# Kernel tuning notes

Measured on AMD Instinct MI355X. Metric: run time of the kernel, lower is better.

Reference implementation:

```python
import jax, jax.numpy as jnp
import numpy as np

def setup_inputs() -> dict:
    key = jax.random.key(0)
    k1, k2, k3 = jax.random.split(key, 3)
    N, G, D = 500000, 10000, 128
    n_embedding = jax.random.normal(k1, (N, D), dtype=jnp.float32)
    g_embedding = jax.random.normal(k2, (G, D), dtype=jnp.float32)
    n_batch = jnp.sort(jax.random.randint(k3, (N,), 0, G, dtype=jnp.int64))
    return {"n_embedding": n_embedding, "g_embedding": g_embedding,
            "n_batch": n_batch, "size": G}

def reference(n_embedding, g_embedding, n_batch, size):
    # gather graph embedding per node: [N, D]
    g_per_node = g_embedding[n_batch]
    # sigmoid of per-node dot product: [N]
    coefs = jax.nn.sigmoid(jnp.sum(n_embedding * g_per_node, axis=1))
    # weighted nodes scatter-added into per-graph pooled output: [G, D]
    weighted = coefs[:, None] * n_embedding
    return jax.ops.segment_sum(weighted, n_batch, num_segments=size)
```

## Files before the change

### kernel.cpp

```cpp
#include <hip/hip_runtime.h>
#include <math.h>


#define BLOCK_THREADS 256
#define GRID_BLOCKS   2048
#define U 4

__global__ __launch_bounds__(BLOCK_THREADS)
void n2g_attention_kernel(const float* __restrict__ n_emb,
                          const float* __restrict__ g_emb,
                          const int*   __restrict__ n_batch,
                          float* __restrict__ out,
                          int N)
{
    const int hw_in_block = threadIdx.x >> 5;
    const int hw_id       = blockIdx.x * (BLOCK_THREADS >> 5) + hw_in_block;
    const int l32         = threadIdx.x & 31;
    const int col         = l32 * 4;
    const int num_hw      = GRID_BLOCKS * (BLOCK_THREADS >> 5);

    const int per   = (N + num_hw - 1) / num_hw;
    const int start = hw_id * per;
    const int end   = min(start + per, N);
    if (start >= N) return;

    float4 acc = make_float4(0.f, 0.f, 0.f, 0.f);
    int cur_g = n_batch[start];

    int i = start;

    for (; i + U <= end; i += U) {
        int    gj[U];
        float4 nv[U], gv[U];

        #pragma unroll
        for (int j = 0; j < U; ++j) gj[j] = n_batch[i + j];
        #pragma unroll
        for (int j = 0; j < U; ++j)
            nv[j] = *(const float4*)(n_emb + (size_t)(i + j) * 128 + col);
        #pragma unroll
        for (int j = 0; j < U; ++j)
            gv[j] = *(const float4*)(g_emb + (size_t)gj[j] * 128 + col);

        float d[U];
        #pragma unroll
        for (int j = 0; j < U; ++j)
            d[j] = nv[j].x * gv[j].x + nv[j].y * gv[j].y
                 + nv[j].z * gv[j].z + nv[j].w * gv[j].w;

        #pragma unroll
        for (int m = 1; m <= 16; m <<= 1) {
            #pragma unroll
            for (int j = 0; j < U; ++j)
                d[j] += __shfl_xor(d[j], m, 64);
        }

        #pragma unroll
        for (int j = 0; j < U; ++j) {
            const float c = 1.0f / (1.0f + __expf(-d[j]));
            if (gj[j] != cur_g) {
                atomicAdd(&out[(size_t)cur_g * 128 + col + 0], acc.x);
                atomicAdd(&out[(size_t)cur_g * 128 + col + 1], acc.y);
                atomicAdd(&out[(size_t)cur_g * 128 + col + 2], acc.z);
                atomicAdd(&out[(size_t)cur_g * 128 + col + 3], acc.w);
                acc = make_float4(0.f, 0.f, 0.f, 0.f);
                cur_g = gj[j];
            }
            acc.x += c * nv[j].x;
            acc.y += c * nv[j].y;
            acc.z += c * nv[j].z;
            acc.w += c * nv[j].w;
        }
    }

    for (; i < end; ++i) {
        const int g = n_batch[i];
        const float4 nv = *(const float4*)(n_emb + (size_t)i * 128 + col);
        const float4 gv = *(const float4*)(g_emb + (size_t)g * 128 + col);
        float d = nv.x * gv.x + nv.y * gv.y + nv.z * gv.z + nv.w * gv.w;
        #pragma unroll
        for (int m = 1; m <= 16; m <<= 1)
            d += __shfl_xor(d, m, 64);
        const float c = 1.0f / (1.0f + __expf(-d));
        if (g != cur_g) {
            atomicAdd(&out[(size_t)cur_g * 128 + col + 0], acc.x);
            atomicAdd(&out[(size_t)cur_g * 128 + col + 1], acc.y);
            atomicAdd(&out[(size_t)cur_g * 128 + col + 2], acc.z);
            atomicAdd(&out[(size_t)cur_g * 128 + col + 3], acc.w);
            acc = make_float4(0.f, 0.f, 0.f, 0.f);
            cur_g = g;
        }
        acc.x += c * nv.x;
        acc.y += c * nv.y;
        acc.z += c * nv.z;
        acc.w += c * nv.w;
    }

    atomicAdd(&out[(size_t)cur_g * 128 + col + 0], acc.x);
    atomicAdd(&out[(size_t)cur_g * 128 + col + 1], acc.y);
    atomicAdd(&out[(size_t)cur_g * 128 + col + 2], acc.z);
    atomicAdd(&out[(size_t)cur_g * 128 + col + 3], acc.w);
}

extern "C" void kernel_launch(void* const* d_in, const int* in_sizes, int n_in,
                              void* d_out, int out_size, void* d_ws, size_t ws_size,
                              hipStream_t stream) {
    const float* n_emb   = (const float*)d_in[0];
    const float* g_emb   = (const float*)d_in[1];
    const int*   n_batch = (const int*)d_in[2];
    float* out = (float*)d_out;
    const int N = in_sizes[2];

    hipMemsetAsync(d_out, 0, (size_t)out_size * sizeof(float), stream);

    n2g_attention_kernel<<<GRID_BLOCKS, BLOCK_THREADS, 0, stream>>>(
        n_emb, g_emb, n_batch, out, N);
}
```

Baseline: 362.6 us.

## Cache graph embedding in registers and add fast path for uniform segments

Keeps the current graph's embedding slice in registers and reloads it only when the segment id changes, so the per-node gather from g_emb goes away. Loads eight batch ids at once with int4 vector loads and rounds the per-half-wave chunk up to a multiple of eight. When the last id in the group matches the current segment, the whole group takes a branch-free batched path; otherwise it falls back to a serial per-node path with a separate shuffle reduction per node. The fallback serialises the shuffle reductions, and U=8 raises register pressure.

After: 355.3 us. -2.0%, faster.

```diff
diff --git a/kernel.cpp b/kernel.cpp
--- a/kernel.cpp
+++ b/kernel.cpp
@@ -4,7 +4,11 @@
 
 #define BLOCK_THREADS 256
 #define GRID_BLOCKS   2048
-#define U 4
+#define U 8
+
+__device__ __forceinline__ float dot4(float4 a, float4 b) {
+    return a.x * b.x + a.y * b.y + a.z * b.z + a.w * b.w;
+}
 
 __global__ __launch_bounds__(BLOCK_THREADS)
 void n2g_attention_kernel(const float* __restrict__ n_emb,
@@ -13,75 +17,77 @@
                           float* __restrict__ out,
                           int N)
 {
-    const int hw_in_block = threadIdx.x >> 5;
-    const int hw_id       = blockIdx.x * (BLOCK_THREADS >> 5) + hw_in_block;
-    const int l32         = threadIdx.x & 31;
-    const int col         = l32 * 4;
-    const int num_hw      = GRID_BLOCKS * (BLOCK_THREADS >> 5);
+    const int hw_id  = blockIdx.x * (BLOCK_THREADS >> 5) + (threadIdx.x >> 5);
+    const int l32    = threadIdx.x & 31;
+    const int col    = l32 * 4;
+    const int num_hw = GRID_BLOCKS * (BLOCK_THREADS >> 5);
 
-    const int per   = (N + num_hw - 1) / num_hw;
+    int per = (N + num_hw - 1) / num_hw;
+    per = (per + U - 1) & ~(U - 1);
     const int start = hw_id * per;
-    const int end   = min(start + per, N);
     if (start >= N) return;
+    const int end = min(start + per, N);
 
     float4 acc = make_float4(0.f, 0.f, 0.f, 0.f);
-    int cur_g = n_batch[start];
+    int    cur_g = n_batch[start];
+    float4 gv = *(const float4*)(g_emb + (size_t)cur_g * 128 + col);
 
     int i = start;
+    for (; i + U <= end; i += U) {
+        const int4 b0 = *(const int4*)(n_batch + i);
+        const int4 b1 = *(const int4*)(n_batch + i + 4);
 
-    for (; i + U <= end; i += U) {
-        int    gj[U];
-        float4 nv[U], gv[U];
-
-        #pragma unroll
-        for (int j = 0; j < U; ++j) gj[j] = n_batch[i + j];
+        float4 nv[U];
         #pragma unroll
         for (int j = 0; j < U; ++j)
             nv[j] = *(const float4*)(n_emb + (size_t)(i + j) * 128 + col);
-        #pragma unroll
-        for (int j = 0; j < U; ++j)
-            gv[j] = *(const float4*)(g_emb + (size_t)gj[j] * 128 + col);
 
-        float d[U];
-        #pragma unroll
-        for (int j = 0; j < U; ++j)
-            d[j] = nv[j].x * gv[j].x + nv[j].y * gv[j].y
-                 + nv[j].z * gv[j].z + nv[j].w * gv[j].w;
+        if (b1.w == cur_g) {
+            float d[U];
+            #pragma unroll
+            for (int j = 0; j < U; ++j) d[j] = dot4(nv[j], gv);
 
-        #pragma unroll
-        for (int m = 1; m <= 16; m <<= 1) {
             #pragma unroll
-            for (int j = 0; j < U; ++j)
-                d[j] += __shfl_xor(d[j], m, 64);
-        }
+            for (int m = 1; m <= 16; m <<= 1) {
+                #pragma unroll
+                for (int j = 0; j < U; ++j) d[j] += __shfl_xor(d[j], m, 64);
+            }
 
-        #pragma unroll
-        for (int j = 0; j < U; ++j) {
-            const float c = 1.0f / (1.0f + __expf(-d[j]));
-            if (gj[j] != cur_g) {
-                atomicAdd(&out[(size_t)cur_g * 128 + col + 0], acc.x);
-                atomicAdd(&out[(size_t)cur_g * 128 + col + 1], acc.y);
-                atomicAdd(&out[(size_t)cur_g * 128 + col + 2], acc.z);
-                atomicAdd(&out[(size_t)cur_g * 128 + col + 3], acc.w);
-                acc = make_float4(0.f, 0.f, 0.f, 0.f);
-                cur_g = gj[j];
+            #pragma unroll
+            for (int j = 0; j < U; ++j) {
+                const float c = 1.0f / (1.0f + __expf(-d[j]));
+                acc.x += c * nv[j].x;
+                acc.y += c * nv[j].y;
+                acc.z += c * nv[j].z;
+                acc.w += c * nv[j].w;
             }
-            acc.x += c * nv[j].x;
-            acc.y += c * nv[j].y;
-            acc.z += c * nv[j].z;
-            acc.w += c * nv[j].w;
+        } else {
+            const int b[U] = {b0.x, b0.y, b0.z, b0.w, b1.x, b1.y, b1.z, b1.w};
+            #pragma unroll
+            for (int j = 0; j < U; ++j) {
+                if (b[j] != cur_g) {
+                    atomicAdd(&out[(size_t)cur_g * 128 + col + 0], acc.x);
+                    atomicAdd(&out[(size_t)cur_g * 128 + col + 1], acc.y);
+                    atomicAdd(&out[(size_t)cur_g * 128 + col + 2], acc.z);
+                    atomicAdd(&out[(size_t)cur_g * 128 + col + 3], acc.w);
+                    acc = make_float4(0.f, 0.f, 0.f, 0.f);
+                    cur_g = b[j];
+                    gv = *(const float4*)(g_emb + (size_t)cur_g * 128 + col);
+                }
+                float d = dot4(nv[j], gv);
+                #pragma unroll
+                for (int m = 1; m <= 16; m <<= 1) d += __shfl_xor(d, m, 64);
+                const float c = 1.0f / (1.0f + __expf(-d));
+                acc.x += c * nv[j].x;
+                acc.y += c * nv[j].y;
+                acc.z += c * nv[j].z;
+                acc.w += c * nv[j].w;
+            }
         }
     }
 
     for (; i < end; ++i) {
         const int g = n_batch[i];
-        const float4 nv = *(const float4*)(n_emb + (size_t)i * 128 + col);
-        const float4 gv = *(const float4*)(g_emb + (size_t)g * 128 + col);
-        float d = nv.x * gv.x + nv.y * gv.y + nv.z * gv.z + nv.w * gv.w;
-        #pragma unroll
-        for (int m = 1; m <= 16; m <<= 1)
-            d += __shfl_xor(d, m, 64);
-        const float c = 1.0f / (1.0f + __expf(-d));
         if (g != cur_g) {
             atomicAdd(&out[(size_t)cur_g * 128 + col + 0], acc.x);
             atomicAdd(&out[(size_t)cur_g * 128 + col + 1], acc.y);
@@ -89,7 +95,13 @@
             atomicAdd(&out[(size_t)cur_g * 128 + col + 3], acc.w);
             acc = make_float4(0.f, 0.f, 0.f, 0.f);
             cur_g = g;
+            gv = *(const float4*)(g_emb + (size_t)cur_g * 128 + col);
         }
+        const float4 nv = *(const float4*)(n_emb + (size_t)i * 128 + col);
+        float d = dot4(nv, gv);
+        #pragma unroll
+        for (int m = 1; m <= 16; m <<= 1) d += __shfl_xor(d, m, 64);
+        const float c = 1.0f / (1.0f + __expf(-d));
         acc.x += c * nv.x;
         acc.y += c * nv.y;
         acc.z += c * nv.z;
```
